# Kernel optimization log

Hardware: AMD Instinct MI355X
Metric: run time of the kernel (lower is better)

The kernel has to match this reference:

```python
import jax, jax.numpy as jnp
import numpy as np

# Module hyperparameters (from init_kwargs)
MANHATTAN_WEIGHTS = jnp.asarray([1.0, 1.0, 2.0], dtype=jnp.float32)  # per-xyz weights
R = 0.4       # density radius
ALPHA = 1.0   # density exponent


def setup_inputs() -> dict:
    key = jax.random.key(0)
    k1, k2 = jax.random.split(key)
    B, N, C = 4, 8192, 16
    points = jax.random.normal(k1, (B, N, 3), dtype=jnp.float32)
    features = jax.random.normal(k2, (B, C, N), dtype=jnp.float32)
    return {"points": points, "features": features, "npoint": 2048}


def reference(points, features, npoint):
    """Density + Manhattan weighted furthest point sampling.

    points:   [B, N, 3] xyz coordinates
    features: [B, C, N] (unused by the sampler, kept for API parity)
    returns:  [B, npoint] int32 sampled indices
    """
    B, N, _ = points.shape
    w = MANHATTAN_WEIGHTS.astype(points.dtype)

    # Per-point density: number of neighbors within Euclidean radius R. [B, N]
    d2 = jnp.sum((points[:, :, None, :] - points[:, None, :, :]) ** 2, axis=-1)  # [B,N,N]
    density = jnp.sum(d2 <= R * R, axis=-1).astype(points.dtype)  # >= 1 (includes self)
    penalty = density ** (-ALPHA)  # low-density points get boosted distance

    def step(carry, _):
        min_dist, cur = carry  # [B,N], [B]
        # coordinates of most recently selected point: [B, 1, 3]
        p = jnp.take_along_axis(points, cur[:, None, None].astype(jnp.int32), axis=1)
        # weighted Manhattan distance of every point to the new sample: [B, N]
        d = jnp.sum(w * jnp.abs(points - p), axis=-1)
        min_dist = jnp.minimum(min_dist, d)
        # fused density-weighted furthest-point criterion
        nxt = jnp.argmax(min_dist * penalty, axis=-1).astype(jnp.int32)
        return (min_dist, nxt), cur

    init = (jnp.full((B, N), 1e10, dtype=points.dtype), jnp.zeros((B,), dtype=jnp.int32))
    _, idx = jax.lax.scan(step, init, None, length=npoint)  # idx: [npoint, B]
    return jnp.transpose(idx)  # [B, npoint]
```

## Files before the change

kernel.cpp:

```cpp
#include <hip/hip_runtime.h>


#define NPTS 8192
#define DENS_BLOCK 256
#define FPS_THREADS 512
#define FPS_P 16


__global__ void dfps_density_kernel(const float* __restrict__ pts,
                                    float* __restrict__ pen, int N) {
#pragma clang fp contract(off)
    const float R2 = (float)(0.4 * 0.4);
    const int b = blockIdx.y;
    const int i = blockIdx.x * blockDim.x + threadIdx.x;
    const float* P = pts + (size_t)b * N * 3;

    __shared__ float sx[DENS_BLOCK], sy[DENS_BLOCK], sz[DENS_BLOCK];

    const float px = P[i * 3 + 0], py = P[i * 3 + 1], pz = P[i * 3 + 2];

    int cnt = 0;
    for (int t0 = 0; t0 < N; t0 += DENS_BLOCK) {
        int j = t0 + threadIdx.x;
        __syncthreads();
        sx[threadIdx.x] = P[j * 3 + 0];
        sy[threadIdx.x] = P[j * 3 + 1];
        sz[threadIdx.x] = P[j * 3 + 2];
        __syncthreads();
#pragma unroll 4
        for (int jj = 0; jj < DENS_BLOCK; ++jj) {
            float dx = px - sx[jj];
            float dy = py - sy[jj];
            float dz = pz - sz[jj];
            float d2 = dx * dx;
            d2 = d2 + dy * dy;
            d2 = d2 + dz * dz;
            cnt += (d2 <= R2) ? 1 : 0;
        }
    }
    pen[(size_t)b * N + i] = 1.0f / (float)cnt;
}


#define DPP_STEP(ctrl, rmask)                                                   \
    {                                                                           \
        unsigned int nlo = (unsigned int)__builtin_amdgcn_update_dpp(           \
            0, (int)klo, (ctrl), (rmask), 0xF, false);                          \
        unsigned int nhi = (unsigned int)__builtin_amdgcn_update_dpp(           \
            0, (int)khi, (ctrl), (rmask), 0xF, false);                          \
        unsigned long long o = ((unsigned long long)nhi << 32) | nlo;           \
        unsigned long long c = ((unsigned long long)khi << 32) | klo;           \
        if (o > c) { klo = nlo; khi = nhi; }                                    \
    }

__global__ void __launch_bounds__(FPS_THREADS, 1)
dfps_fps_kernel(const float* __restrict__ pts,
                const float* __restrict__ penalty,
                const int* __restrict__ npoint_p,
                int* __restrict__ out, int N) {
#pragma clang fp contract(off)
    const int b = blockIdx.x;
    const int tid = threadIdx.x;
    const int lane = tid & 63;
    const int npoint = *npoint_p;
    const float* Pb = pts + (size_t)b * N * 3;
    const float* pen = penalty + (size_t)b * N;
    const int base = tid * FPS_P;

    __shared__ float4 tab[NPTS];
    __shared__ unsigned long long slot[3];

    float x[FPS_P], y[FPS_P], z[FPS_P], md[FPS_P], pw[FPS_P];
    unsigned int lo[FPS_P];
#pragma unroll
    for (int k = 0; k < FPS_P; ++k) {
        int idx = base + k;
        x[k] = Pb[idx * 3 + 0];
        y[k] = Pb[idx * 3 + 1];
        z[k] = Pb[idx * 3 + 2];
        md[k] = 1e10f;
        pw[k] = pen[idx];
        lo[k] = (unsigned int)(N - 1 - idx);
        tab[idx] = make_float4(x[k], y[k], z[k], 0.f);
    }
    if (tid == 0) { slot[0] = 0ull; slot[2] = 0ull; }
    __syncthreads();

    int cur = 0;
    float cx = Pb[0], cy = Pb[1], cz = Pb[2];

    for (int t = 0; t < npoint; ++t) {
        if (tid == 0) {
            out[(size_t)b * npoint + t] = cur;
            slot[(t + 1) % 3] = 0ull;
        }

        unsigned long long ck0 = 0ull, ck1 = 0ull, ck2 = 0ull, ck3 = 0ull;
#pragma unroll
        for (int k = 0; k < FPS_P; ++k) {
            float d = fabsf(x[k] - cx) + fabsf(y[k] - cy);
            d = fmaf(2.0f, fabsf(z[k] - cz), d);
            float m = fminf(md[k], d);
            md[k] = m;
            float v = m * pw[k];
            unsigned long long key =
                ((unsigned long long)__float_as_uint(v) << 32) | lo[k];
            if ((k & 3) == 0)      { if (key > ck0) ck0 = key; }
            else if ((k & 3) == 1) { if (key > ck1) ck1 = key; }
            else if ((k & 3) == 2) { if (key > ck2) ck2 = key; }
            else                   { if (key > ck3) ck3 = key; }
        }
        unsigned long long ka = ck0 > ck1 ? ck0 : ck1;
        unsigned long long kb = ck2 > ck3 ? ck2 : ck3;
        unsigned long long best = ka > kb ? ka : kb;

        unsigned int klo = (unsigned int)best;
        unsigned int khi = (unsigned int)(best >> 32);
        DPP_STEP(0x111, 0xF)
        DPP_STEP(0x112, 0xF)
        DPP_STEP(0x114, 0xF)
        DPP_STEP(0x118, 0xF)
        DPP_STEP(0x142, 0xA)
        DPP_STEP(0x143, 0xC)

        if (lane == 63) {
            unsigned long long wk = ((unsigned long long)khi << 32) | klo;
            atomicMax(&slot[t % 3], wk);
        }
        __syncthreads();

        unsigned long long bk = slot[t % 3];
        cur = (N - 1) - (int)(unsigned int)(bk & 0xFFFFFFFFull);
        float4 c = tab[cur];
        cx = c.x;
        cy = c.y;
        cz = c.z;
    }
}

extern "C" void kernel_launch(void* const* d_in, const int* in_sizes, int n_in,
                              void* d_out, int out_size, void* d_ws, size_t ws_size,
                              hipStream_t stream) {
    const float* points  = (const float*)d_in[0];
    const int*   npoint  = (const int*)d_in[2];
    int* out = (int*)d_out;

    const int B = 4;
    const int N = in_sizes[0] / (B * 3);
    float* penalty = (float*)d_ws;

    dim3 dgrid(N / DENS_BLOCK, B);
    dfps_density_kernel<<<dgrid, DENS_BLOCK, 0, stream>>>(points, penalty, N);

    dfps_fps_kernel<<<B, FPS_THREADS, 0, stream>>>(points, penalty, npoint, out, N);
}
```

Baseline: 2.051 ms.

## Split density count across blocks and pack FPS math into float2 vectors

The density kernel now splits the neighbor range into four slices over a third grid dimension. Each slice writes a partial count, and the FPS kernel sums the four counts and inverts them at load time. The density kernel drops its shared-memory tiling and reads neighbor coordinates directly from global memory, two at a time, using packed float2 arithmetic. The FPS inner loop packs coordinate differences and the penalty multiply into v2f operations to try to use packed FP32 instructions, and the per-step output write and slot reset move to different waves. The extra partial-count workspace and the uncached global reads in the density pass are the tradeoffs.

Measured after the change: 2.129 ms. 1.04x slower.

```diff
diff --git a/kernel.cpp b/kernel.cpp
--- a/kernel.cpp
+++ b/kernel.cpp
@@ -3,42 +3,46 @@
 
 #define NPTS 8192
 #define DENS_BLOCK 256
+#define DENS_SPLIT 4
 #define FPS_THREADS 512
 #define FPS_P 16
+#define FPS_P2 (FPS_P / 2)
+
+typedef float v2f __attribute__((ext_vector_type(2)));
 
 
-__global__ void dfps_density_kernel(const float* __restrict__ pts,
-                                    float* __restrict__ pen, int N) {
+__global__ void dfps_density_partial(const float* __restrict__ pts,
+                                     float* __restrict__ pen4, int N) {
 #pragma clang fp contract(off)
     const float R2 = (float)(0.4 * 0.4);
     const int b = blockIdx.y;
+    const int z = blockIdx.z;
     const int i = blockIdx.x * blockDim.x + threadIdx.x;
     const float* P = pts + (size_t)b * N * 3;
 
-    __shared__ float sx[DENS_BLOCK], sy[DENS_BLOCK], sz[DENS_BLOCK];
+    const v2f px2 = {P[i * 3 + 0], P[i * 3 + 0]};
+    const v2f py2 = {P[i * 3 + 1], P[i * 3 + 1]};
+    const v2f pz2 = {P[i * 3 + 2], P[i * 3 + 2]};
 
-    const float px = P[i * 3 + 0], py = P[i * 3 + 1], pz = P[i * 3 + 2];
+    const int j0 = z * (N / DENS_SPLIT);
+    const int j1 = j0 + (N / DENS_SPLIT);
 
     int cnt = 0;
-    for (int t0 = 0; t0 < N; t0 += DENS_BLOCK) {
-        int j = t0 + threadIdx.x;
-        __syncthreads();
-        sx[threadIdx.x] = P[j * 3 + 0];
-        sy[threadIdx.x] = P[j * 3 + 1];
-        sz[threadIdx.x] = P[j * 3 + 2];
-        __syncthreads();
 #pragma unroll 4
-        for (int jj = 0; jj < DENS_BLOCK; ++jj) {
-            float dx = px - sx[jj];
-            float dy = py - sy[jj];
-            float dz = pz - sz[jj];
-            float d2 = dx * dx;
-            d2 = d2 + dy * dy;
-            d2 = d2 + dz * dz;
-            cnt += (d2 <= R2) ? 1 : 0;
-        }
+    for (int j = j0; j < j1; j += 2) {
+        v2f qx = {P[3 * j + 0], P[3 * j + 3]};
+        v2f qy = {P[3 * j + 1], P[3 * j + 4]};
+        v2f qz = {P[3 * j + 2], P[3 * j + 5]};
+        v2f dx = px2 - qx;
+        v2f dy = py2 - qy;
+        v2f dz = pz2 - qz;
+        v2f d2 = dx * dx;
+        d2 = d2 + dy * dy;
+        d2 = d2 + dz * dz;
+        cnt += (d2.x <= R2) ? 1 : 0;
+        cnt += (d2.y <= R2) ? 1 : 0;
     }
-    pen[(size_t)b * N + i] = 1.0f / (float)cnt;
+    pen4[(size_t)(z * 4 + b) * N + i] = (float)cnt;
 }
 
 
@@ -55,7 +59,7 @@
 
 __global__ void __launch_bounds__(FPS_THREADS, 1)
 dfps_fps_kernel(const float* __restrict__ pts,
-                const float* __restrict__ penalty,
+                const float* __restrict__ pen4,
                 const int* __restrict__ npoint_p,
                 int* __restrict__ out, int N) {
 #pragma clang fp contract(off)
@@ -64,24 +68,31 @@
     const int lane = tid & 63;
     const int npoint = *npoint_p;
     const float* Pb = pts + (size_t)b * N * 3;
-    const float* pen = penalty + (size_t)b * N;
     const int base = tid * FPS_P;
 
     __shared__ float4 tab[NPTS];
     __shared__ unsigned long long slot[3];
 
-    float x[FPS_P], y[FPS_P], z[FPS_P], md[FPS_P], pw[FPS_P];
+    v2f xp[FPS_P2], yp[FPS_P2], zp[FPS_P2], mdp[FPS_P2], pwp[FPS_P2];
     unsigned int lo[FPS_P];
 #pragma unroll
-    for (int k = 0; k < FPS_P; ++k) {
-        int idx = base + k;
-        x[k] = Pb[idx * 3 + 0];
-        y[k] = Pb[idx * 3 + 1];
-        z[k] = Pb[idx * 3 + 2];
-        md[k] = 1e10f;
-        pw[k] = pen[idx];
-        lo[k] = (unsigned int)(N - 1 - idx);
-        tab[idx] = make_float4(x[k], y[k], z[k], 0.f);
+    for (int j = 0; j < FPS_P2; ++j) {
+        int idx = base + 2 * j;
+        float x0 = Pb[idx * 3 + 0], y0 = Pb[idx * 3 + 1], z0 = Pb[idx * 3 + 2];
+        float x1 = Pb[idx * 3 + 3], y1 = Pb[idx * 3 + 4], z1 = Pb[idx * 3 + 5];
+        xp[j] = (v2f){x0, x1};
+        yp[j] = (v2f){y0, y1};
+        zp[j] = (v2f){z0, z1};
+        mdp[j] = (v2f){1e10f, 1e10f};
+        float c0 = pen4[(size_t)(0 * 4 + b) * N + idx]     + pen4[(size_t)(1 * 4 + b) * N + idx];
+        float c1 = pen4[(size_t)(2 * 4 + b) * N + idx]     + pen4[(size_t)(3 * 4 + b) * N + idx];
+        float e0 = pen4[(size_t)(0 * 4 + b) * N + idx + 1] + pen4[(size_t)(1 * 4 + b) * N + idx + 1];
+        float e1 = pen4[(size_t)(2 * 4 + b) * N + idx + 1] + pen4[(size_t)(3 * 4 + b) * N + idx + 1];
+        pwp[j] = (v2f){1.0f / (c0 + c1), 1.0f / (e0 + e1)};
+        lo[2 * j]     = (unsigned int)(N - 1 - idx);
+        lo[2 * j + 1] = (unsigned int)(N - 1 - (idx + 1));
+        tab[idx]     = make_float4(x0, y0, z0, 0.f);
+        tab[idx + 1] = make_float4(x1, y1, z1, 0.f);
     }
     if (tid == 0) { slot[0] = 0ull; slot[2] = 0ull; }
     __syncthreads();
@@ -90,25 +101,37 @@
     float cx = Pb[0], cy = Pb[1], cz = Pb[2];
 
     for (int t = 0; t < npoint; ++t) {
-        if (tid == 0) {
-            out[(size_t)b * npoint + t] = cur;
-            slot[(t + 1) % 3] = 0ull;
-        }
+        if (tid == 64) out[(size_t)b * npoint + t] = cur;
+        if (tid == 128) slot[(t + 1) % 3] = 0ull;
+
+        const v2f cx2 = {cx, cx}, cy2 = {cy, cy}, cz2 = {cz, cz};
 
         unsigned long long ck0 = 0ull, ck1 = 0ull, ck2 = 0ull, ck3 = 0ull;
 #pragma unroll
-        for (int k = 0; k < FPS_P; ++k) {
-            float d = fabsf(x[k] - cx) + fabsf(y[k] - cy);
-            d = fmaf(2.0f, fabsf(z[k] - cz), d);
-            float m = fminf(md[k], d);
-            md[k] = m;
-            float v = m * pw[k];
-            unsigned long long key =
-                ((unsigned long long)__float_as_uint(v) << 32) | lo[k];
-            if ((k & 3) == 0)      { if (key > ck0) ck0 = key; }
-            else if ((k & 3) == 1) { if (key > ck1) ck1 = key; }
-            else if ((k & 3) == 2) { if (key > ck2) ck2 = key; }
-            else                   { if (key > ck3) ck3 = key; }
+        for (int j = 0; j < FPS_P2; ++j) {
+            v2f dx = xp[j] - cx2;
+            v2f dy = yp[j] - cy2;
+            v2f dz = zp[j] - cz2;
+            float d0 = fabsf(dx.x) + fabsf(dy.x);
+            float d1 = fabsf(dx.y) + fabsf(dy.y);
+            d0 = fmaf(2.0f, fabsf(dz.x), d0);
+            d1 = fmaf(2.0f, fabsf(dz.y), d1);
+            v2f m;
+            m.x = fminf(mdp[j].x, d0);
+            m.y = fminf(mdp[j].y, d1);
+            mdp[j] = m;
+            v2f v = m * pwp[j];
+            unsigned long long k0 =
+                ((unsigned long long)__float_as_uint(v.x) << 32) | lo[2 * j];
+            unsigned long long k1 =
+                ((unsigned long long)__float_as_uint(v.y) << 32) | lo[2 * j + 1];
+            if (j & 1) {
+                if (k0 > ck2) ck2 = k0;
+                if (k1 > ck3) ck3 = k1;
+            } else {
+                if (k0 > ck0) ck0 = k0;
+                if (k1 > ck1) ck1 = k1;
+            }
         }
         unsigned long long ka = ck0 > ck1 ? ck0 : ck1;
         unsigned long long kb = ck2 > ck3 ? ck2 : ck3;
@@ -147,10 +170,10 @@
 
     const int B = 4;
     const int N = in_sizes[0] / (B * 3);
-    float* penalty = (float*)d_ws;
+    float* pen4 = (float*)d_ws;
 
-    dim3 dgrid(N / DENS_BLOCK, B);
-    dfps_density_kernel<<<dgrid, DENS_BLOCK, 0, stream>>>(points, penalty, N);
+    dim3 dgrid(N / DENS_BLOCK, B, DENS_SPLIT);
+    dfps_density_partial<<<dgrid, DENS_BLOCK, 0, stream>>>(points, pen4, N);
 
-    dfps_fps_kernel<<<B, FPS_THREADS, 0, stream>>>(points, penalty, npoint, out, N);
+    dfps_fps_kernel<<<B, FPS_THREADS, 0, stream>>>(points, pen4, npoint, out, N);
 }
```

## Split density count across blocks, use packed float math, widen FPS block

Applied to the files above, without the earlier changes.

The density kernel is split four ways over the neighbor range, producing partial counts that the FPS kernel sums and inverts at load time. It drops shared-memory staging in favor of direct global (cached) loads and processes two neighbors at once with float2 vector ops. The FPS kernel moves from 512 threads with 16 points each to 1024 threads with 8 points each, giving shorter per-thread work but more waves to combine at each barrier. Workspace grows to four partial-count arrays, and summation order is still exact because the counts are small integers.

New measurement: 2.234 ms. 8.9% more time.

```diff
diff --git a/kernel.cpp b/kernel.cpp
--- a/kernel.cpp
+++ b/kernel.cpp
@@ -3,42 +3,45 @@
 
 #define NPTS 8192
 #define DENS_BLOCK 256
-#define FPS_THREADS 512
-#define FPS_P 16
+#define DENS_SPLIT 4
+#define FPS_THREADS 1024
+#define FPS_P 8
+
+typedef float v2f __attribute__((ext_vector_type(2)));
 
 
-__global__ void dfps_density_kernel(const float* __restrict__ pts,
-                                    float* __restrict__ pen, int N) {
+__global__ void dfps_density_partial(const float* __restrict__ pts,
+                                     float* __restrict__ pen4, int N) {
 #pragma clang fp contract(off)
     const float R2 = (float)(0.4 * 0.4);
     const int b = blockIdx.y;
+    const int z = blockIdx.z;
     const int i = blockIdx.x * blockDim.x + threadIdx.x;
     const float* P = pts + (size_t)b * N * 3;
 
-    __shared__ float sx[DENS_BLOCK], sy[DENS_BLOCK], sz[DENS_BLOCK];
+    const v2f px2 = {P[i * 3 + 0], P[i * 3 + 0]};
+    const v2f py2 = {P[i * 3 + 1], P[i * 3 + 1]};
+    const v2f pz2 = {P[i * 3 + 2], P[i * 3 + 2]};
 
-    const float px = P[i * 3 + 0], py = P[i * 3 + 1], pz = P[i * 3 + 2];
+    const int j0 = z * (N / DENS_SPLIT);
+    const int j1 = j0 + (N / DENS_SPLIT);
 
     int cnt = 0;
-    for (int t0 = 0; t0 < N; t0 += DENS_BLOCK) {
-        int j = t0 + threadIdx.x;
-        __syncthreads();
-        sx[threadIdx.x] = P[j * 3 + 0];
-        sy[threadIdx.x] = P[j * 3 + 1];
-        sz[threadIdx.x] = P[j * 3 + 2];
-        __syncthreads();
 #pragma unroll 4
-        for (int jj = 0; jj < DENS_BLOCK; ++jj) {
-            float dx = px - sx[jj];
-            float dy = py - sy[jj];
-            float dz = pz - sz[jj];
-            float d2 = dx * dx;
-            d2 = d2 + dy * dy;
-            d2 = d2 + dz * dz;
-            cnt += (d2 <= R2) ? 1 : 0;
-        }
+    for (int j = j0; j < j1; j += 2) {
+        v2f qx = {P[3 * j + 0], P[3 * j + 3]};
+        v2f qy = {P[3 * j + 1], P[3 * j + 4]};
+        v2f qz = {P[3 * j + 2], P[3 * j + 5]};
+        v2f dx = px2 - qx;
+        v2f dy = py2 - qy;
+        v2f dz = pz2 - qz;
+        v2f d2 = dx * dx;
+        d2 = d2 + dy * dy;
+        d2 = d2 + dz * dz;
+        cnt += (d2.x <= R2) ? 1 : 0;
+        cnt += (d2.y <= R2) ? 1 : 0;
     }
-    pen[(size_t)b * N + i] = 1.0f / (float)cnt;
+    pen4[(size_t)(z * 4 + b) * N + i] = (float)cnt;
 }
 
 
@@ -55,7 +58,7 @@
 
 __global__ void __launch_bounds__(FPS_THREADS, 1)
 dfps_fps_kernel(const float* __restrict__ pts,
-                const float* __restrict__ penalty,
+                const float* __restrict__ pen4,
                 const int* __restrict__ npoint_p,
                 int* __restrict__ out, int N) {
 #pragma clang fp contract(off)
@@ -64,7 +67,6 @@
     const int lane = tid & 63;
     const int npoint = *npoint_p;
     const float* Pb = pts + (size_t)b * N * 3;
-    const float* pen = penalty + (size_t)b * N;
     const int base = tid * FPS_P;
 
     __shared__ float4 tab[NPTS];
@@ -79,7 +81,11 @@
         y[k] = Pb[idx * 3 + 1];
         z[k] = Pb[idx * 3 + 2];
         md[k] = 1e10f;
-        pw[k] = pen[idx];
+        float c01 = pen4[(size_t)(0 * 4 + b) * N + idx] +
+                    pen4[(size_t)(1 * 4 + b) * N + idx];
+        float c23 = pen4[(size_t)(2 * 4 + b) * N + idx] +
+                    pen4[(size_t)(3 * 4 + b) * N + idx];
+        pw[k] = 1.0f / (c01 + c23);
         lo[k] = (unsigned int)(N - 1 - idx);
         tab[idx] = make_float4(x[k], y[k], z[k], 0.f);
     }
@@ -147,10 +153,10 @@
 
     const int B = 4;
     const int N = in_sizes[0] / (B * 3);
-    float* penalty = (float*)d_ws;
+    float* pen4 = (float*)d_ws;
 
-    dim3 dgrid(N / DENS_BLOCK, B);
-    dfps_density_kernel<<<dgrid, DENS_BLOCK, 0, stream>>>(points, penalty, N);
+    dim3 dgrid(N / DENS_BLOCK, B, DENS_SPLIT);
+    dfps_density_partial<<<dgrid, DENS_BLOCK, 0, stream>>>(points, pen4, N);
 
-    dfps_fps_kernel<<<B, FPS_THREADS, 0, stream>>>(points, penalty, npoint, out, N);
+    dfps_fps_kernel<<<B, FPS_THREADS, 0, stream>>>(points, pen4, npoint, out, N);
 }
```
